# Performance work log

Hardware: AMD Instinct MI355X
Metric: run time of the kernel (lower is better)

## Reference

```python
import jax, jax.numpy as jnp
import numpy as np
import math

B, T, C, H = 4, 2048, 1024, 16
D = C // H  # head dim = 64


def setup_inputs() -> dict:
    key = jax.random.key(0)
    ks = jax.random.split(key, 5)
    scale = 0.02
    x = jax.random.normal(ks[0], (B, T, C), dtype=jnp.float32)
    # torch nn.Linear(n_embd, 3*n_embd): weight [3C, C]; we store transposed [C, 3C]
    W_kqv = jax.random.normal(ks[1], (C, 3 * C), dtype=jnp.float32) * scale
    b_kqv = jnp.zeros((3 * C,), dtype=jnp.float32)
    W_proj = jax.random.normal(ks[2], (C, C), dtype=jnp.float32) * scale
    b_proj = jnp.zeros((C,), dtype=jnp.float32)
    padding_mask = jnp.ones((B, T), dtype=jnp.int32)  # 1 = valid token
    return {"x": x, "W_kqv": W_kqv, "b_kqv": b_kqv, "W_proj": W_proj,
            "b_proj": b_proj, "padding_mask": padding_mask}


def reference(x, W_kqv, b_kqv, W_proj, b_proj, padding_mask):
    Bx, Tx, Cx = x.shape
    kqv = x @ W_kqv + b_kqv                      # [B,T,3C]
    # original splits as k, q, v (in that order)
    k, q, v = jnp.split(kqv, 3, axis=2)
    def heads(t):
        return t.reshape(Bx, Tx, H, D).transpose(0, 2, 1, 3)  # [B,H,T,D]
    k, q, v = heads(k), heads(q), heads(v)
    att = jnp.einsum('bhqd,bhkd->bhqk', q, k) * (1.0 / math.sqrt(D))  # [B,H,T,T]
    causal = jnp.tril(jnp.ones((Tx, Tx), dtype=bool))[None, None]     # [1,1,T,T]
    valid = causal & (padding_mask[:, None, None, :] != 0)            # [B,1,T,T] broadcast
    neg_inf = jnp.finfo(att.dtype).min
    att = jnp.where(valid, att, neg_inf)
    att = jax.nn.softmax(att, axis=-1)
    y = jnp.einsum('bhqk,bhkd->bhqd', att, v)    # [B,H,T,D]
    y = y.transpose(0, 2, 1, 3).reshape(Bx, Tx, Cx)
    return y @ W_proj + b_proj
```

## Files before the change

kernel.cpp:

```cpp
#include <hip/hip_runtime.h>


typedef short bf16x8 __attribute__((ext_vector_type(8)));
typedef float floatx4 __attribute__((ext_vector_type(4)));

#define MFMA16(a, b, c) __builtin_amdgcn_mfma_f32_16x16x32_bf16(a, b, c, 0, 0, 0)

#define ASYNC_COPY16(gp, lp)                                                   \
  __builtin_amdgcn_global_load_lds(                                            \
      (__attribute__((address_space(1))) void*)(gp),                           \
      (__attribute__((address_space(3))) void*)(lp), 16, 0, 0)

#define DRAIN_VMCNT() asm volatile("s_waitcnt vmcnt(0)" ::: "memory")

#if defined(__has_builtin)
#if __has_builtin(__builtin_amdgcn_exp2f)
#define EXP2(x) __builtin_amdgcn_exp2f(x)
#endif
#endif
#ifndef EXP2
#define EXP2(x) exp2f(x)
#endif

__device__ __forceinline__ short f2bf(float f) {
  union { float f; unsigned u; } c;
  c.f = f;
  unsigned r = c.u + 0x7fffu + ((c.u >> 16) & 1u);
  return (short)(r >> 16);
}

__global__ __launch_bounds__(256) void cvt_f32_bf16(const float* __restrict__ in,
                                                    short* __restrict__ out) {
  int i = (blockIdx.x * 256 + threadIdx.x) * 4;
  float4 v = *(const float4*)&in[i];
  short4 o;
  o.x = f2bf(v.x); o.y = f2bf(v.y); o.z = f2bf(v.z); o.w = f2bf(v.w);
  *(short4*)&out[i] = o;
}

__global__ __launch_bounds__(256) void pmb_kernel(const int* __restrict__ pm,
                                                  float* __restrict__ pmbf) {
  int i = blockIdx.x * 256 + threadIdx.x;
  pmbf[i] = pm[i] ? 0.0f : -3.0e38f;
}

__global__ __launch_bounds__(256) void transpose_cvt_tiled(const float* __restrict__ in,
                                                           short* __restrict__ out,
                                                           int N) {
  __shared__ float buf[64][65];
  const int t = threadIdx.x;
  const int k0 = blockIdx.y * 64, n0 = blockIdx.x * 64;
#pragma unroll
  for (int i = 0; i < 4; ++i) {
    int s = t + i * 256;
    int row = s >> 4, c4 = (s & 15) * 4;
    float4 v = *(const float4*)&in[(size_t)(k0 + row) * N + n0 + c4];
    buf[row][c4] = v.x; buf[row][c4 + 1] = v.y;
    buf[row][c4 + 2] = v.z; buf[row][c4 + 3] = v.w;
  }
  __syncthreads();
#pragma unroll
  for (int i = 0; i < 2; ++i) {
    int u = t + i * 256;
    int rn = u >> 3, ch = (u & 7) * 8;
    short tmp[8];
#pragma unroll
    for (int j = 0; j < 8; ++j) tmp[j] = f2bf(buf[ch + j][rn]);
    *(uint4*)&out[(size_t)(n0 + rn) * 1024 + k0 + ch] = *(uint4*)tmp;
  }
}

template <int MODE>
__global__ __launch_bounds__(256) void gemm_bt128(const short* __restrict__ A,
                                                  const short* __restrict__ Bt,
                                                  const float* __restrict__ bias,
                                                  void* __restrict__ Cout,
                                                  int M, int N, int K) {
  __shared__ short smem[128 * 136];
  short* As = smem;
  short* Bs = smem + 8192;
  const int tid = threadIdx.x;
  const int lane = tid & 63;
  const int wv = tid >> 6;
  const int l15 = lane & 15, quad = lane >> 4;
  const int xr = l15 & 7;
  const int m0 = blockIdx.y * 128, n0 = blockIdx.x * 128;
  const int wm = (wv >> 1) * 64, wn = (wv & 1) * 64;

  floatx4 acc[4][4] = {};

  const int srow = tid >> 3;
  const int gch = ((tid & 7) ^ (srow & 7)) * 8;

  const short* Ap = &A[(size_t)(m0 + srow) * K + gch];
  const short* Bp = &Bt[(size_t)(n0 + srow) * K + gch];
  short* Asp = &As[tid * 8];
  short* Bsp = &Bs[tid * 8];

  for (int k0 = 0; k0 < K; k0 += 64) {
#pragma unroll
    for (int i = 0; i < 4; ++i) {
      ASYNC_COPY16(Ap + (size_t)(i * 32) * K + k0, Asp + i * 2048);
      ASYNC_COPY16(Bp + (size_t)(i * 32) * K + k0, Bsp + i * 2048);
    }
    DRAIN_VMCNT();
    __syncthreads();
#pragma unroll
    for (int s = 0; s < 2; ++s) {
      const int chs = ((s * 4 + quad) ^ xr) * 8;
      bf16x8 af[4], bfr[4];
#pragma unroll
      for (int i = 0; i < 4; ++i) {
        af[i]  = *(const bf16x8*)&As[(wm + i * 16 + l15) * 64 + chs];
        bfr[i] = *(const bf16x8*)&Bs[(wn + i * 16 + l15) * 64 + chs];
      }
#pragma unroll
      for (int mi = 0; mi < 4; ++mi)
#pragma unroll
        for (int ni = 0; ni < 4; ++ni)
          acc[mi][ni] = MFMA16(af[mi], bfr[ni], acc[mi][ni]);
    }
    __syncthreads();
  }

  if (MODE == 0) {
    float* outf = (float*)Cout;
#pragma unroll
    for (int ni = 0; ni < 4; ++ni) {
      int col = n0 + wn + ni * 16 + l15;
      float bv = bias[col];
#pragma unroll
      for (int mi = 0; mi < 4; ++mi) {
#pragma unroll
        for (int rr = 0; rr < 4; ++rr) {
          int row = m0 + wm + mi * 16 + quad * 4 + rr;
          outf[(size_t)row * N + col] = acc[mi][ni][rr] + bv;
        }
      }
    }
  } else {
    short* outs = (short*)Cout;
    const size_t QOFF = (size_t)64 * 2048 * 64;
    const int sec = n0 >> 10;
#pragma unroll
    for (int ni = 0; ni < 4; ++ni) {
      int c = wn + ni * 16 + l15;
      float bv = bias[n0 + c];
#pragma unroll
      for (int mi = 0; mi < 4; ++mi) {
        int r0 = wm + mi * 16 + quad * 4;
#pragma unroll
        for (int rr = 0; rr < 4; ++rr) {
          short v = f2bf(acc[mi][ni][rr] + bv);
          if (sec < 2) smem[(r0 + rr) * 136 + c] = v;
          else         smem[c * 136 + (r0 + rr)] = v;
        }
      }
    }
    __syncthreads();
#pragma unroll
    for (int j = 0; j < 8; ++j) {
      int idx = j * 256 + tid;
      int rr2 = idx >> 4;
      int cc2 = (idx & 15) * 8;
      uint4 v = *(const uint4*)&smem[rr2 * 136 + cc2];
      if (sec < 2) {
        int colg = n0 + cc2;
        int hh = (colg >> 6) & 15, dd = colg & 63;
        int row = m0 + rr2, bb = row >> 11, tt = row & 2047;
        *(uint4*)(outs + (size_t)sec * QOFF +
                  (((size_t)(bb * 16 + hh) * 2048 + tt) * 64 + dd)) = v;
      } else {
        int colg = n0 + rr2;
        int hh = (colg >> 6) & 15, dd = colg & 63;
        int row = m0 + cc2, bb = row >> 11, tt = row & 2047;
        *(uint4*)(outs + 2 * QOFF +
                  ((size_t)(bb * 16 + hh) * 64 + dd) * 2048 + tt) = v;
      }
    }
  }
}

__global__ __launch_bounds__(256, 3) void attn_flash7(const short* __restrict__ Qd,
                                                      const short* __restrict__ Kd,
                                                      const short* __restrict__ Vd,
                                                      const float* __restrict__ pmbf,
                                                      short* __restrict__ y) {
  constexpr int T = 2048, C = 1024;
  __shared__ short Ks[128 * 64];
  __shared__ short Vs[64 * 128];
  __shared__ short Ps[4][32][64];

  const int tid = threadIdx.x;
  const int lane = tid & 63, w = tid >> 6;
  const int l15 = lane & 15, quad = lane >> 4;
  const int xr = l15 & 7;
  const int lin = blockIdx.x;
  const int qb = 15 - (lin >> 6);
  const int bh = lin & 63;
  const int b = bh >> 4, h = bh & 15;
  const short* Qb = Qd + (size_t)bh * T * 64;
  const short* Kb = Kd + (size_t)bh * T * 64;
  const short* Vb = Vd + (size_t)bh * 64 * T;
  const float* pmb = &pmbf[b * T];
  const int q0 = qb * 128;

  const float SCALE2 = 0.18033688011112042f;

  bf16x8 qf[2][2];
#pragma unroll
  for (int mi = 0; mi < 2; ++mi) {
    const short* qp = Qb + (size_t)(q0 + w * 32 + mi * 16 + l15) * 64;
    qf[mi][0] = *(const bf16x8*)&qp[quad * 8];
    qf[mi][1] = *(const bf16x8*)&qp[32 + quad * 8];
  }

  floatx4 Oacc[2][4] = {};
  float lpart[2] = {};

#pragma unroll 1
  for (int k0 = 0; k0 <= q0; k0 += 128) {
    {
      const short* ksrc = Kb + (size_t)k0 * 64;
      const short* vsrc = Vb + k0;
#pragma unroll
      for (int j = 0; j < 4; ++j) {
        int c = j * 256 + tid;
        int krow = c >> 3, kc = (c & 7) ^ (krow & 7);
        ASYNC_COPY16(ksrc + krow * 64 + kc * 8, &Ks[c * 8]);
        int vrow = c >> 4, vc = (c & 15) ^ (vrow & 7);
        ASYNC_COPY16(vsrc + (size_t)vrow * T + vc * 8, &Vs[c * 8]);
      }
    }
    DRAIN_VMCNT();
    __syncthreads();

    const bool diag = (k0 == q0);

#pragma unroll
    for (int kh = 0; kh < 2; ++kh) {
      floatx4 Sacc[2][4] = {};
#pragma unroll
      for (int s = 0; s < 2; ++s) {
#pragma unroll
        for (int n4 = 0; n4 < 4; ++n4) {
          bf16x8 bK = *(const bf16x8*)
              &Ks[((kh * 4 + n4) * 16 + l15) * 64 + (((s * 4 + quad) ^ xr) * 8)];
          Sacc[0][n4] = MFMA16(bK, qf[0][s], Sacc[0][n4]);
          Sacc[1][n4] = MFMA16(bK, qf[1][s], Sacc[1][n4]);
        }
      }

      if (!diag) {
#pragma unroll
        for (int n4 = 0; n4 < 4; ++n4) {
          floatx4 pb4 = *(const floatx4*)&pmb[k0 + kh * 64 + n4 * 16 + quad * 4];
#pragma unroll
          for (int mi = 0; mi < 2; ++mi) {
            float p[4];
#pragma unroll
            for (int rr = 0; rr < 4; ++rr) {
              p[rr] = EXP2(fmaf(Sacc[mi][n4][rr], SCALE2, pb4[rr]));
              lpart[mi] += p[rr];
            }
            unsigned lo, hi;
            asm("v_cvt_pk_bf16_f32 %0, %1, %2" : "=v"(lo) : "v"(p[0]), "v"(p[1]));
            asm("v_cvt_pk_bf16_f32 %0, %1, %2" : "=v"(hi) : "v"(p[2]), "v"(p[3]));
            uint2 pk; pk.x = lo; pk.y = hi;
            *(uint2*)&Ps[w][mi * 16 + l15]
                        [((n4 * 2 + (quad >> 1)) ^ xr) * 8 + (quad & 1) * 4] = pk;
          }
        }
      } else {
#pragma unroll
        for (int n4 = 0; n4 < 4; ++n4) {
          floatx4 pb4 = *(const floatx4*)&pmb[k0 + kh * 64 + n4 * 16 + quad * 4];
          const int colb = kh * 64 + n4 * 16 + quad * 4;
#pragma unroll
          for (int mi = 0; mi < 2; ++mi) {
            const int rowb = w * 32 + mi * 16 + l15;
            float p[4];
#pragma unroll
            for (int rr = 0; rr < 4; ++rr) {
              float v = EXP2(fmaf(Sacc[mi][n4][rr], SCALE2, pb4[rr]));
              if (colb + rr > rowb) v = 0.f;
              p[rr] = v;
              lpart[mi] += v;
            }
            unsigned lo, hi;
            asm("v_cvt_pk_bf16_f32 %0, %1, %2" : "=v"(lo) : "v"(p[0]), "v"(p[1]));
            asm("v_cvt_pk_bf16_f32 %0, %1, %2" : "=v"(hi) : "v"(p[2]), "v"(p[3]));
            uint2 pk; pk.x = lo; pk.y = hi;
            *(uint2*)&Ps[w][mi * 16 + l15]
                        [((n4 * 2 + (quad >> 1)) ^ xr) * 8 + (quad & 1) * 4] = pk;
          }
        }
      }

#pragma unroll
      for (int ks2 = 0; ks2 < 2; ++ks2) {
        const int pco = (((ks2 * 4 + quad) ^ xr) * 8);
        bf16x8 ap0 = *(const bf16x8*)&Ps[w][l15][pco];
        bf16x8 ap1 = *(const bf16x8*)&Ps[w][16 + l15][pco];
#pragma unroll
        for (int nd = 0; nd < 4; ++nd) {
          bf16x8 bV = *(const bf16x8*)
              &Vs[(nd * 16 + l15) * 128 +
                  (((kh * 8 + ks2 * 4 + quad) ^ xr) * 8)];
          Oacc[0][nd] = MFMA16(ap0, bV, Oacc[0][nd]);
          Oacc[1][nd] = MFMA16(ap1, bV, Oacc[1][nd]);
        }
      }
    }
    __syncthreads();
  }

#pragma unroll
  for (int mi = 0; mi < 2; ++mi) {
    float s = lpart[mi];
    s += __shfl_xor(s, 16, 64);
    s += __shfl_xor(s, 32, 64);
    float inv_l[4];
#pragma unroll
    for (int rr = 0; rr < 4; ++rr)
      inv_l[rr] = 1.0f / __shfl(s, quad * 4 + rr, 16);
#pragma unroll
    for (int n = 0; n < 4; ++n) {
      int dcol = n * 16 + l15;
#pragma unroll
      for (int rr = 0; rr < 4; ++rr) {
        int rowq = q0 + w * 32 + mi * 16 + quad * 4 + rr;
        y[((size_t)(b * T + rowq)) * C + h * 64 + dcol] =
            f2bf(Oacc[mi][n][rr] * inv_l[rr]);
      }
    }
  }
}

extern "C" void kernel_launch(void* const* d_in, const int* in_sizes, int n_in,
                              void* d_out, int out_size, void* d_ws, size_t ws_size,
                              hipStream_t stream) {
  constexpr int B = 4, T = 2048, C = 1024;
  constexpr int M = B * T;
  constexpr int N1 = 3 * C;

  const float* x      = (const float*)d_in[0];
  const float* W_kqv  = (const float*)d_in[1];
  const float* b_kqv  = (const float*)d_in[2];
  const float* W_proj = (const float*)d_in[3];
  const float* b_proj = (const float*)d_in[4];
  const int*   pmask  = (const int*)d_in[5];
  float* out = (float*)d_out;

  const size_t QOFF = (size_t)64 * T * 64;

  short* xb     = (short*)d_ws;
  short* Wkqvt  = xb + (size_t)M * C;
  short* Wprojt = Wkqvt + (size_t)N1 * C;
  short* qkv    = Wprojt + (size_t)C * C;
  float* pmbf   = (float*)(qkv + 3 * QOFF);
  short* yb     = xb;

  short* Kd = qkv;
  short* Qd = qkv + QOFF;
  short* Vd = qkv + 2 * QOFF;

  cvt_f32_bf16<<<(M * C) / (256 * 4), 256, 0, stream>>>(x, xb);
  transpose_cvt_tiled<<<dim3(N1 / 64, 16), 256, 0, stream>>>(W_kqv, Wkqvt, N1);
  transpose_cvt_tiled<<<dim3(C / 64, 16), 256, 0, stream>>>(W_proj, Wprojt, C);
  pmb_kernel<<<(B * T) / 256, 256, 0, stream>>>(pmask, pmbf);

  gemm_bt128<2><<<dim3(N1 / 128, M / 128), 256, 0, stream>>>(xb, Wkqvt, b_kqv, Kd, M, N1, C);

  attn_flash7<<<dim3(1024), 256, 0, stream>>>(Qd, Kd, Vd, pmbf, yb);

  gemm_bt128<0><<<dim3(C / 128, M / 128), 256, 0, stream>>>(yb, Wprojt, b_proj, out, M, C, C);
}
```

Before: 258.5 us.

## Double-buffer K/V in 64-key tiles to overlap loads with attention compute

```diff
diff --git a/kernel.cpp b/kernel.cpp
--- a/kernel.cpp
+++ b/kernel.cpp
@@ -181,14 +181,14 @@
   }
 }
 
-__global__ __launch_bounds__(256, 3) void attn_flash7(const short* __restrict__ Qd,
+__global__ __launch_bounds__(256, 3) void attn_flash8(const short* __restrict__ Qd,
                                                       const short* __restrict__ Kd,
                                                       const short* __restrict__ Vd,
                                                       const float* __restrict__ pmbf,
                                                       short* __restrict__ y) {
   constexpr int T = 2048, C = 1024;
-  __shared__ short Ks[128 * 64];
-  __shared__ short Vs[64 * 128];
+  __shared__ short Ks[2][64 * 64];
+  __shared__ short Vs[2][64 * 64];
   __shared__ short Ps[4][32][64];
 
   const int tid = threadIdx.x;
@@ -204,8 +204,22 @@
   const short* Vb = Vd + (size_t)bh * 64 * T;
   const float* pmb = &pmbf[b * T];
   const int q0 = qb * 128;
+  const int nt = (q0 >> 6) + 2;
 
   const float SCALE2 = 0.18033688011112042f;
+
+#define STAGE_KV(t, buf)                                                       \
+  {                                                                            \
+    const short* ksrc_ = Kb + (size_t)((t) * 64) * 64;                         \
+    const short* vsrc_ = Vb + (t) * 64;                                        \
+    _Pragma("unroll")                                                          \
+    for (int j_ = 0; j_ < 2; ++j_) {                                           \
+      int c_ = j_ * 256 + tid;                                                 \
+      int r_ = c_ >> 3, cc_ = (c_ & 7) ^ (r_ & 7);                             \
+      ASYNC_COPY16(ksrc_ + r_ * 64 + cc_ * 8, &Ks[buf][c_ * 8]);               \
+      ASYNC_COPY16(vsrc_ + (size_t)r_ * T + cc_ * 8, &Vs[buf][c_ * 8]);        \
+    }                                                                          \
+  }
 
   bf16x8 qf[2][2];
 #pragma unroll
@@ -218,102 +232,93 @@
   floatx4 Oacc[2][4] = {};
   float lpart[2] = {};
 
+  STAGE_KV(0, 0);
+  DRAIN_VMCNT();
+  __syncthreads();
+
+  int cur = 0;
 #pragma unroll 1
-  for (int k0 = 0; k0 <= q0; k0 += 128) {
-    {
-      const short* ksrc = Kb + (size_t)k0 * 64;
-      const short* vsrc = Vb + k0;
-#pragma unroll
-      for (int j = 0; j < 4; ++j) {
-        int c = j * 256 + tid;
-        int krow = c >> 3, kc = (c & 7) ^ (krow & 7);
-        ASYNC_COPY16(ksrc + krow * 64 + kc * 8, &Ks[c * 8]);
-        int vrow = c >> 4, vc = (c & 15) ^ (vrow & 7);
-        ASYNC_COPY16(vsrc + (size_t)vrow * T + vc * 8, &Vs[c * 8]);
-      }
-    }
+  for (int t = 0; t < nt; ++t) {
+    const int k0 = t * 64;
+    if (t + 1 < nt) STAGE_KV(t + 1, cur ^ 1);
+
+    floatx4 Sacc[2][4] = {};
+#pragma unroll
+    for (int s = 0; s < 2; ++s) {
+#pragma unroll
+      for (int n4 = 0; n4 < 4; ++n4) {
+        bf16x8 bK = *(const bf16x8*)
+            &Ks[cur][(n4 * 16 + l15) * 64 + (((s * 4 + quad) ^ xr) * 8)];
+        Sacc[0][n4] = MFMA16(bK, qf[0][s], Sacc[0][n4]);
+        Sacc[1][n4] = MFMA16(bK, qf[1][s], Sacc[1][n4]);
+      }
+    }
+
+    if (k0 < q0) {
+#pragma unroll
+      for (int n4 = 0; n4 < 4; ++n4) {
+        floatx4 pb4 = *(const floatx4*)&pmb[k0 + n4 * 16 + quad * 4];
+#pragma unroll
+        for (int mi = 0; mi < 2; ++mi) {
+          float p[4];
+#pragma unroll
+          for (int rr = 0; rr < 4; ++rr) {
+            p[rr] = EXP2(fmaf(Sacc[mi][n4][rr], SCALE2, pb4[rr]));
+            lpart[mi] += p[rr];
+          }
+          unsigned lo, hi;
+          asm("v_cvt_pk_bf16_f32 %0, %1, %2" : "=v"(lo) : "v"(p[0]), "v"(p[1]));
+          asm("v_cvt_pk_bf16_f32 %0, %1, %2" : "=v"(hi) : "v"(p[2]), "v"(p[3]));
+          uint2 pk; pk.x = lo; pk.y = hi;
+          *(uint2*)&Ps[w][mi * 16 + l15]
+                      [((n4 * 2 + (quad >> 1)) ^ xr) * 8 + (quad & 1) * 4] = pk;
+        }
+      }
+    } else {
+#pragma unroll
+      for (int n4 = 0; n4 < 4; ++n4) {
+        floatx4 pb4 = *(const floatx4*)&pmb[k0 + n4 * 16 + quad * 4];
+        const int colb = n4 * 16 + quad * 4;
+#pragma unroll
+        for (int mi = 0; mi < 2; ++mi) {
+          const int rowb = (q0 - k0) + w * 32 + mi * 16 + l15;
+          float p[4];
+#pragma unroll
+          for (int rr = 0; rr < 4; ++rr) {
+            float v = EXP2(fmaf(Sacc[mi][n4][rr], SCALE2, pb4[rr]));
+            if (colb + rr > rowb) v = 0.f;
+            p[rr] = v;
+            lpart[mi] += v;
+          }
+          unsigned lo, hi;
+          asm("v_cvt_pk_bf16_f32 %0, %1, %2" : "=v"(lo) : "v"(p[0]), "v"(p[1]));
+          asm("v_cvt_pk_bf16_f32 %0, %1, %2" : "=v"(hi) : "v"(p[2]), "v"(p[3]));
+          uint2 pk; pk.x = lo; pk.y = hi;
+          *(uint2*)&Ps[w][mi * 16 + l15]
+                      [((n4 * 2 + (quad >> 1)) ^ xr) * 8 + (quad & 1) * 4] = pk;
+        }
+      }
+    }
+
+#pragma unroll
+    for (int ks2 = 0; ks2 < 2; ++ks2) {
+      const int pco = (((ks2 * 4 + quad) ^ xr) * 8);
+      bf16x8 ap0 = *(const bf16x8*)&Ps[w][l15][pco];
+      bf16x8 ap1 = *(const bf16x8*)&Ps[w][16 + l15][pco];
+#pragma unroll
+      for (int nd = 0; nd < 4; ++nd) {
+        bf16x8 bV = *(const bf16x8*)
+            &Vs[cur][(nd * 16 + l15) * 64 + (((ks2 * 4 + quad) ^ xr) * 8)];
+        Oacc[0][nd] = MFMA16(ap0, bV, Oacc[0][nd]);
+        Oacc[1][nd] = MFMA16(ap1, bV, Oacc[1][nd]);
+      }
+    }
+
     DRAIN_VMCNT();
     __syncthreads();
-
-    const bool diag = (k0 == q0);
-
-#pragma unroll
-    for (int kh = 0; kh < 2; ++kh) {
-      floatx4 Sacc[2][4] = {};
-#pragma unroll
-      for (int s = 0; s < 2; ++s) {
-#pragma unroll
-        for (int n4 = 0; n4 < 4; ++n4) {
-          bf16x8 bK = *(const bf16x8*)
-              &Ks[((kh * 4 + n4) * 16 + l15) * 64 + (((s * 4 + quad) ^ xr) * 8)];
-          Sacc[0][n4] = MFMA16(bK, qf[0][s], Sacc[0][n4]);
-          Sacc[1][n4] = MFMA16(bK, qf[1][s], Sacc[1][n4]);
-        }
-      }
-
-      if (!diag) {
-#pragma unroll
-        for (int n4 = 0; n4 < 4; ++n4) {
-          floatx4 pb4 = *(const floatx4*)&pmb[k0 + kh * 64 + n4 * 16 + quad * 4];
-#pragma unroll
-          for (int mi = 0; mi < 2; ++mi) {
-            float p[4];
-#pragma unroll
-            for (int rr = 0; rr < 4; ++rr) {
-              p[rr] = EXP2(fmaf(Sacc[mi][n4][rr], SCALE2, pb4[rr]));
-              lpart[mi] += p[rr];
-            }
-            unsigned lo, hi;
-            asm("v_cvt_pk_bf16_f32 %0, %1, %2" : "=v"(lo) : "v"(p[0]), "v"(p[1]));
-            asm("v_cvt_pk_bf16_f32 %0, %1, %2" : "=v"(hi) : "v"(p[2]), "v"(p[3]));
-            uint2 pk; pk.x = lo; pk.y = hi;
-            *(uint2*)&Ps[w][mi * 16 + l15]
-                        [((n4 * 2 + (quad >> 1)) ^ xr) * 8 + (quad & 1) * 4] = pk;
-          }
-        }
-      } else {
-#pragma unroll
-        for (int n4 = 0; n4 < 4; ++n4) {
-          floatx4 pb4 = *(const floatx4*)&pmb[k0 + kh * 64 + n4 * 16 + quad * 4];
-          const int colb = kh * 64 + n4 * 16 + quad * 4;
-#pragma unroll
-          for (int mi = 0; mi < 2; ++mi) {
-            const int rowb = w * 32 + mi * 16 + l15;
-            float p[4];
-#pragma unroll
-            for (int rr = 0; rr < 4; ++rr) {
-              float v = EXP2(fmaf(Sacc[mi][n4][rr], SCALE2, pb4[rr]));
-              if (colb + rr > rowb) v = 0.f;
-              p[rr] = v;
-              lpart[mi] += v;
-            }
-            unsigned lo, hi;
-            asm("v_cvt_pk_bf16_f32 %0, %1, %2" : "=v"(lo) : "v"(p[0]), "v"(p[1]));
-            asm("v_cvt_pk_bf16_f32 %0, %1, %2" : "=v"(hi) : "v"(p[2]), "v"(p[3]));
-            uint2 pk; pk.x = lo; pk.y = hi;
-            *(uint2*)&Ps[w][mi * 16 + l15]
-                        [((n4 * 2 + (quad >> 1)) ^ xr) * 8 + (quad & 1) * 4] = pk;
-          }
-        }
-      }
-
-#pragma unroll
-      for (int ks2 = 0; ks2 < 2; ++ks2) {
-        const int pco = (((ks2 * 4 + quad) ^ xr) * 8);
-        bf16x8 ap0 = *(const bf16x8*)&Ps[w][l15][pco];
-        bf16x8 ap1 = *(const bf16x8*)&Ps[w][16 + l15][pco];
-#pragma unroll
-        for (int nd = 0; nd < 4; ++nd) {
-          bf16x8 bV = *(const bf16x8*)
-              &Vs[(nd * 16 + l15) * 128 +
-                  (((kh * 8 + ks2 * 4 + quad) ^ xr) * 8)];
-          Oacc[0][nd] = MFMA16(ap0, bV, Oacc[0][nd]);
-          Oacc[1][nd] = MFMA16(ap1, bV, Oacc[1][nd]);
-        }
-      }
-    }
-    __syncthreads();
-  }
+    cur ^= 1;
+  }
+#undef STAGE_KV
 
 #pragma unroll
   for (int mi = 0; mi < 2; ++mi) {
@@ -372,7 +377,7 @@
 
   gemm_bt128<2><<<dim3(N1 / 128, M / 128), 256, 0, stream>>>(xb, Wkqvt, b_kqv, Kd, M, N1, C);
 
-  attn_flash7<<<dim3(1024), 256, 0, stream>>>(Qd, Kd, Vd, pmbf, yb);
+  attn_flash8<<<dim3(1024), 256, 0, stream>>>(Qd, Kd, Vd, pmbf, yb);
 
   gemm_bt128<0><<<dim3(C / 128, M / 128), 256, 0, stream>>>(yb, Wprojt, b_proj, out, M, C, C);
 }
```

Result: no change. 254.6 us (-1.5%).
